# Kernel tuning notes

Measured on AMD Instinct MI355X. Metric: run time of the kernel, lower is better.

Reference implementation:

```python
import jax, jax.numpy as jnp
import numpy as np

E = 32          # n_routed_experts / num_local_experts
H = 1024        # hidden_size
I = 512         # moe_intermediate_size
G = 8           # n_group
TKG = 4         # topk_group
TOPK = 8        # num_experts_per_tok
NSH = 2         # n_shared_experts
SCALE = 2.5     # routed_scaling_factor


def setup_inputs() -> dict:
    key = jax.random.key(0)
    ks = jax.random.split(key, 10)
    s = 0.02
    return {
        "hidden_states": jax.random.normal(ks[0], (2, 1024, H), jnp.float32),
        # router: linear weight [E, H] and e_score_correction_bias [E]
        "gate_w": jax.random.normal(ks[1], (E, H), jnp.float32) * s,
        "gate_bias": jax.random.normal(ks[2], (E,), jnp.float32) * s,
        # routed experts (stacked SwiGLU weights, torch Linear layout [out, in])
        "w_gate": jax.random.normal(ks[3], (E, I, H), jnp.float32) * s,
        "w_up": jax.random.normal(ks[4], (E, I, H), jnp.float32) * s,
        "w_down": jax.random.normal(ks[5], (E, H, I), jnp.float32) * s,
        # shared experts: one MLP with intermediate = I * NSH
        "sh_gate": jax.random.normal(ks[6], (I * NSH, H), jnp.float32) * s,
        "sh_up": jax.random.normal(ks[7], (I * NSH, H), jnp.float32) * s,
        "sh_down": jax.random.normal(ks[8], (H, I * NSH), jnp.float32) * s,
    }


def reference(hidden_states, gate_w, gate_bias, w_gate, w_up, w_down,
              sh_gate, sh_up, sh_down):
    B, S, Hd = hidden_states.shape
    h = hidden_states.reshape(-1, Hd)                      # [T, H]

    # ---- router (DeepseekV3TopkRouter + route_tokens_to_experts) ----
    logits = h.astype(jnp.float32) @ gate_w.T              # [T, E]
    scores = jax.nn.sigmoid(logits)
    sc = scores + gate_bias                                # scores_for_choice
    # group score = sum of top-2 expert scores within each group
    grp = sc.reshape(-1, G, E // G)                        # [T, G, E/G]
    group_scores = jax.lax.top_k(grp, 2)[0].sum(-1)        # [T, G]
    gidx = jax.lax.top_k(group_scores, TKG)[1]             # [T, TKG]
    gmask = jnp.sum(jax.nn.one_hot(gidx, G, dtype=sc.dtype), axis=1)  # [T, G]
    smask = jnp.repeat(gmask, E // G, axis=1)              # [T, E]
    masked = jnp.where(smask > 0, sc, jnp.zeros_like(sc))  # masked_fill(~mask, 0)
    tki = jax.lax.top_k(masked, TOPK)[1]                   # [T, TOPK]
    tkw = jnp.take_along_axis(scores, tki, axis=1)         # gather raw sigmoid scores
    tkw = tkw / (tkw.sum(-1, keepdims=True) + 1e-20)       # norm_topk_prob
    tkw = tkw * SCALE

    # ---- dispatch-compute-combine (experts_forward) ----
    # combine[t, e] = sum_k tkw[t, k] * [tki[t, k] == e]
    combine = (jax.nn.one_hot(tki, E, dtype=tkw.dtype) * tkw[..., None]).sum(1)  # [T, E]
    g = jax.nn.silu(jnp.einsum('th,eih->tei', h, w_gate))  # [T, E, I]
    u = jnp.einsum('th,eih->tei', h, w_up)                 # [T, E, I]
    routed = jnp.einsum('tei,ehi->th', g * u * combine[:, :, None], w_down)  # [T, H]

    # ---- shared experts ----
    sg = jax.nn.silu(h @ sh_gate.T)
    shared = (sg * (h @ sh_up.T)) @ sh_down.T              # [T, H]

    return (routed + shared).reshape(B, S, Hd)
```

## Files before the change

### kernel.cpp

```cpp
#include <hip/hip_runtime.h>
#include <hip/hip_bf16.h>
#include <cstdint>

#define E_ 32
#define H_ 1024
#define I_ 512
#define G_ 8
#define NSH_ 2
#define SCALE_ 2.5f
#define NROUTED (E_ * I_)
#define PADCAP (16384 + E_ * 128)

typedef unsigned short u16;
using bf16x8_t = __attribute__((ext_vector_type(8))) __bf16;
using f32x4_t  = __attribute__((ext_vector_type(4))) float;

__device__ __forceinline__ u16 f2bf(float x) {
  union { float f; uint32_t u; } v; v.f = x;
  uint32_t u = v.u;
  uint32_t r = (u + 0x7fffu + ((u >> 16) & 1u)) >> 16;
  return (u16)r;
}
__device__ __forceinline__ float bf2f(u16 x) {
  union { uint32_t u; float f; } v; v.u = ((uint32_t)x) << 16; return v.f;
}

__device__ __forceinline__ void load_lds16(const void* g, void* l) {
  __builtin_amdgcn_global_load_lds(
      (const __attribute__((address_space(1))) unsigned int*)g,
      (__attribute__((address_space(3))) unsigned int*)l,
      16, 0, 0);
}

#define OFF_BU   16777216L
#define OFF_BD   33554432L
#define OFF_BSHG 50331648L
#define OFF_BSHU 51380224L
#define OFF_BSHD 52428800L
#define WBF_TOT  53477376L

#define W4_WG  4194304L
#define W4_WU  8388608L
#define W4_WD  12582912L
#define W4_SHG 12845056L
#define W4_SHU 13107200L
#define W4_TOT 13369344L
__global__ void prep_kernel(const float* __restrict__ gw, float* __restrict__ gwT,
                            int* __restrict__ counts, int* __restrict__ cursor,
                            int* __restrict__ qheads,
                            int* __restrict__ tok_list, float* __restrict__ wt_list,
                            const float* __restrict__ wg, const float* __restrict__ wu,
                            const float* __restrict__ wd, const float* __restrict__ shg,
                            const float* __restrict__ shu, const float* __restrict__ shd,
                            u16* __restrict__ wbf) {
  long i0 = (long)blockIdx.x * blockDim.x + threadIdx.x;
  if (i0 < H_ * E_) {
    int k = (int)(i0 >> 5), e = (int)(i0 & 31);
    gwT[i0] = gw[(long)e * H_ + k];
  }
  if (i0 < PADCAP) { tok_list[i0] = 0; wt_list[i0] = 0.f; }
  if (i0 < E_) { counts[i0] = 0; cursor[i0] = 0; }
  if (i0 < 2) qheads[i0] = 0;

  long stride = (long)gridDim.x * blockDim.x;
  for (long i = i0; i < W4_TOT; i += stride) {
    const float* s; long off; long dofs;
    if (i < W4_WG)       { s = wg;  off = i;            dofs = off * 4; }
    else if (i < W4_WU)  { s = wu;  off = i - W4_WG;    dofs = OFF_BU + off * 4; }
    else if (i < W4_WD)  { s = wd;  off = i - W4_WU;    dofs = OFF_BD + off * 4; }
    else if (i < W4_SHG) { s = shg; off = i - W4_WD;    dofs = OFF_BSHG + off * 4; }
    else if (i < W4_SHU) { s = shu; off = i - W4_SHG;   dofs = OFF_BSHU + off * 4; }
    else                 { s = shd; off = i - W4_SHU;   dofs = OFF_BSHD + off * 4; }
    float4 v = ((const float4*)s)[off];
    ushort4 o;
    o.x = f2bf(v.x); o.y = f2bf(v.y); o.z = f2bf(v.z); o.w = f2bf(v.w);
    *(ushort4*)(wbf + dofs) = o;
  }
}

__global__ __launch_bounds__(256) void router_kernel(
    const float* __restrict__ h, const float* __restrict__ gwT,
    const float* __restrict__ gb, u16* __restrict__ hbf,
    int* __restrict__ idx8, float* __restrict__ wt8, int* __restrict__ counts) {
  __shared__ float sh[8][H_];
  __shared__ float s_log[8][E_ + 1];
  const int tid = threadIdx.x;
  const int t0 = blockIdx.x * 8;
  #pragma unroll
  for (int c = tid; c < 8 * H_ / 4; c += 256) {
    int row = c / (H_ / 4), col = c % (H_ / 4);
    float4 v = ((const float4*)(h + (size_t)(t0 + row) * H_))[col];
    ((float4*)sh[row])[col] = v;
    ushort4 o;
    o.x = f2bf(v.x); o.y = f2bf(v.y); o.z = f2bf(v.z); o.w = f2bf(v.w);
    ((ushort4*)(hbf + (size_t)(t0 + row) * H_))[col] = o;
  }
  __syncthreads();
  {
    const int w = tid >> 6, l = tid & 63;
    const int e = l & 31, tl = w * 2 + (l >> 5);
    const float* hp = sh[tl];
    const float* wp = gwT + e;
    float acc = 0.f;
    #pragma unroll 8
    for (int k = 0; k < H_; ++k) acc += hp[k] * wp[(size_t)k * E_];
    s_log[tl][e] = acc;
  }
  __syncthreads();
  if (tid < 8) {
    const int t = t0 + tid;
    float scr[E_], sc[E_];
    #pragma unroll
    for (int e = 0; e < E_; ++e) {
      float sig = 1.f / (1.f + __expf(-s_log[tid][e]));
      scr[e] = sig;
      sc[e] = sig + gb[e];
    }
    float gs[G_];
    #pragma unroll
    for (int g = 0; g < G_; ++g) {
      float a = sc[g * 4], b = sc[g * 4 + 1], c = sc[g * 4 + 2], d = sc[g * 4 + 3];
      float hi1 = fmaxf(a, b), lo1 = fminf(a, b);
      float hi2 = fmaxf(c, d), lo2 = fminf(c, d);
      float m1 = fmaxf(hi1, hi2);
      float m2 = (hi1 >= hi2) ? fmaxf(lo1, hi2) : fmaxf(lo2, hi1);
      gs[g] = m1 + m2;
    }
    unsigned gm = 0;
    #pragma unroll
    for (int r = 0; r < 4; ++r) {
      float bv = -1e30f; int bi = 0;
      #pragma unroll
      for (int g = 0; g < G_; ++g)
        if (!(gm & (1u << g)) && gs[g] > bv) { bv = gs[g]; bi = g; }
      gm |= 1u << bi;
    }
    float msk[E_];
    #pragma unroll
    for (int e = 0; e < E_; ++e)
      msk[e] = ((gm >> (e >> 2)) & 1u) ? sc[e] : 0.f;
    unsigned um = 0; float wsum = 0.f;
    int idxs[8]; float wts[8];
    #pragma unroll
    for (int r = 0; r < 8; ++r) {
      float bv = -1e30f; int bi = 0;
      #pragma unroll
      for (int e = 0; e < E_; ++e)
        if (!(um & (1u << e)) && msk[e] > bv) { bv = msk[e]; bi = e; }
      um |= 1u << bi;
      idxs[r] = bi;
      float wv = scr[bi];
      wts[r] = wv; wsum += wv;
    }
    float inv = SCALE_ / (wsum + 1e-20f);
    #pragma unroll
    for (int r = 0; r < 8; ++r) {
      idx8[(size_t)t * 8 + r] = idxs[r];
      wt8[(size_t)t * 8 + r] = wts[r] * inv;
      atomicAdd(&counts[idxs[r]], 1);
    }
  }
}

__global__ void fill_kernel(const int* __restrict__ idx8, const float* __restrict__ wt8,
                            const int* __restrict__ counts, int* __restrict__ cursor,
                            int* __restrict__ tok_list, float* __restrict__ wt_list,
                            int* __restrict__ pair_pos, int npair) {
  int i = blockIdx.x * blockDim.x + threadIdx.x;
  if (i >= npair) return;
  int e = idx8[i];
  int offz = 0;
  for (int k = 0; k < E_; ++k) {
    if (k == e) break;
    offz += ((counts[k] + 127) >> 7) << 7;
  }
  int p = atomicAdd(&cursor[e], 1);
  int slot = offz + p;
  tok_list[slot] = i >> 3;
  wt_list[slot] = wt8[i];
  pair_pos[i] = slot;
}

__global__ __launch_bounds__(256, 2) void p1_kernel(
    const u16* __restrict__ hbf,
    const u16* __restrict__ wbf,
    const int* __restrict__ counts,
    const int* __restrict__ tok_list, const float* __restrict__ wt_list,
    int* __restrict__ qheads,
    u16* __restrict__ gu,
    u16* __restrict__ gu_sh,
    int T) {
  __shared__ u16 lsA[2][128 * 32];
  __shared__ u16 lsB0[2][128 * 32];
  __shared__ u16 lsB1[2][128 * 32];
  __shared__ int s_tok[128];
  __shared__ float s_wt[128];
  __shared__ int s_off[E_], s_ntt[E_];
  __shared__ int s_tot, s_tile;

  const int tid = threadIdx.x;
  if (tid == 0) {
    int run = 0, tot = 0;
    for (int e = 0; e < E_; ++e) {
      s_off[e] = run;
      int nt = (counts[e] + 127) >> 7;
      s_ntt[e] = nt;
      run += nt << 7;
      tot += nt * 4;
    }
    s_tot = tot + (T / 128) * 8;
  }

  const int w = tid >> 6, l = tid & 63;
  const int wr = w >> 1, wc = w & 1;
  const int lr = l & 15, lh = l >> 4;
  const int rdblk = (lh ^ ((lr >> 1) & 3)) << 3;

  const int c0 = tid, c1 = tid + 256;
  const int row0 = c0 >> 2, cb0 = c0 & 3, scb0 = cb0 ^ ((row0 >> 1) & 3);
  const int row1 = c1 >> 2, cb1 = c1 & 3, scb1 = cb1 ^ ((row1 >> 1) & 3);

  for (;;) {
    __syncthreads();
    if (tid == 0) s_tile = atomicAdd(&qheads[0], 1);
    __syncthreads();
    int q = s_tile;
    if (q >= s_tot) break;

    int z = 0, rem = q;
    for (; z < E_; ++z) { int t = s_ntt[z] * 4; if (rem < t) break; rem -= t; }
    const bool sh_e = (z == E_);
    int tt, nb;
    if (sh_e) { tt = rem >> 3; nb = rem & 7; }
    else      { tt = rem >> 2; nb = rem & 3; }
    const int off = sh_e ? 0 : s_off[z];

    if (tid < 128) {
      if (sh_e) { s_tok[tid] = tt * 128 + tid; s_wt[tid] = 1.0f; }
      else {
        int slot = off + tt * 128 + tid;
        s_tok[tid] = tok_list[slot];
        s_wt[tid] = wt_list[slot];
      }
    }
    __syncthreads();

    const u16* Bg = sh_e ? (wbf + OFF_BSHG + (size_t)(nb * 128) * H_)
                         : (wbf + ((size_t)z * I_ + nb * 128) * H_);
    const u16* Bu = sh_e ? (wbf + OFF_BSHU + (size_t)(nb * 128) * H_)
                         : (wbf + OFF_BU + ((size_t)z * I_ + nb * 128) * H_);
    const u16* A0 = hbf + (size_t)s_tok[row0] * H_ + scb0 * 8;
    const u16* A1 = hbf + (size_t)s_tok[row1] * H_ + scb1 * 8;

    f32x4_t acc0[4][4], acc1[4][4];
    #pragma unroll
    for (int m = 0; m < 4; ++m)
      #pragma unroll
      for (int n = 0; n < 4; ++n) {
        acc0[m][n] = (f32x4_t){0.f, 0.f, 0.f, 0.f};
        acc1[m][n] = (f32x4_t){0.f, 0.f, 0.f, 0.f};
      }

    auto stage = [&](int b, int k0) {
      load_lds16(A0 + k0, (char*)&lsA[b][0] + c0 * 16);
      load_lds16(A1 + k0, (char*)&lsA[b][0] + c1 * 16);
      load_lds16(Bg + (size_t)row0 * H_ + k0 + scb0 * 8, (char*)&lsB0[b][0] + c0 * 16);
      load_lds16(Bg + (size_t)row1 * H_ + k0 + scb1 * 8, (char*)&lsB0[b][0] + c1 * 16);
      load_lds16(Bu + (size_t)row0 * H_ + k0 + scb0 * 8, (char*)&lsB1[b][0] + c0 * 16);
      load_lds16(Bu + (size_t)row1 * H_ + k0 + scb1 * 8, (char*)&lsB1[b][0] + c1 * 16);
    };
    auto compute = [&](int b) {
      bf16x8_t af[4], b0f[4], b1f[4];
      #pragma unroll
      for (int m = 0; m < 4; ++m)
        af[m] = *(const bf16x8_t*)(&lsA[b][0] + (wr * 64 + m * 16 + lr) * 32 + rdblk);
      #pragma unroll
      for (int n = 0; n < 4; ++n) {
        b0f[n] = *(const bf16x8_t*)(&lsB0[b][0] + (wc * 64 + n * 16 + lr) * 32 + rdblk);
        b1f[n] = *(const bf16x8_t*)(&lsB1[b][0] + (wc * 64 + n * 16 + lr) * 32 + rdblk);
      }
      #pragma unroll
      for (int m = 0; m < 4; ++m)
        #pragma unroll
        for (int n = 0; n < 4; ++n) {
          acc0[m][n] = __builtin_amdgcn_mfma_f32_16x16x32_bf16(af[m], b0f[n], acc0[m][n], 0, 0, 0);
          acc1[m][n] = __builtin_amdgcn_mfma_f32_16x16x32_bf16(af[m], b1f[n], acc1[m][n], 0, 0, 0);
        }
    };

    stage(0, 0);
    __syncthreads();
    int cur = 0;
    #pragma unroll 1
    for (int s = 0; s < 32; ++s) {
      if (s < 31) stage(cur ^ 1, (s + 1) * 32);
      compute(cur);
      __syncthreads();
      cur ^= 1;
    }

    const int ldo = sh_e ? (I_ * NSH_) : I_;
    u16* outp = sh_e ? (gu_sh + (size_t)(tt * 128) * ldo + nb * 128)
                     : (gu + (size_t)(off + tt * 128) * ldo + nb * 128);
    #pragma unroll
    for (int m = 0; m < 4; ++m) {
      #pragma unroll
      for (int n = 0; n < 4; ++n) {
        int col = wc * 64 + n * 16 + lr;
        #pragma unroll
        for (int j = 0; j < 4; ++j) {
          int trow = wr * 64 + m * 16 + lh * 4 + j;
          float gv = acc0[m][n][j], uv = acc1[m][n][j];
          float sv = gv / (1.f + __expf(-gv));
          outp[(size_t)trow * ldo + col] = f2bf(sv * uv * s_wt[trow]);
        }
      }
    }
  }
}

__global__ __launch_bounds__(256, 3) void p2_kernel(
    const u16* __restrict__ gu, const u16* __restrict__ gu_sh,
    const u16* __restrict__ wbf,
    const int* __restrict__ counts,
    int* __restrict__ qheads,
    u16* __restrict__ part,
    u16* __restrict__ part_sh,
    int T) {
  __shared__ u16 lsA[2][128 * 32];
  __shared__ u16 lsB[2][128 * 32];
  __shared__ int s_off[E_], s_ntt[E_];
  __shared__ int s_tot, s_tile;

  const int tid = threadIdx.x;
  if (tid == 0) {
    int run = 0, tot = 0;
    for (int e = 0; e < E_; ++e) {
      s_off[e] = run;
      int nt = (counts[e] + 127) >> 7;
      s_ntt[e] = nt;
      run += nt << 7;
      tot += nt * 8;
    }
    s_tot = tot + (T / 128) * 8;
  }

  const int w = tid >> 6, l = tid & 63;
  const int wr = w >> 1, wc = w & 1;
  const int lr = l & 15, lh = l >> 4;
  const int rdblk = (lh ^ ((lr >> 1) & 3)) << 3;

  const int c0 = tid, c1 = tid + 256;
  const int row0 = c0 >> 2, cb0 = c0 & 3, scb0 = cb0 ^ ((row0 >> 1) & 3);
  const int row1 = c1 >> 2, cb1 = c1 & 3, scb1 = cb1 ^ ((row1 >> 1) & 3);

  for (;;) {
    __syncthreads();
    if (tid == 0) s_tile = atomicAdd(&qheads[1], 1);
    __syncthreads();
    int q = s_tile;
    if (q >= s_tot) break;

    int z = 0, rem = q;
    for (; z < E_; ++z) { int t = s_ntt[z] * 8; if (rem < t) break; rem -= t; }
    const bool sh_e = (z == E_);
    int tt = rem >> 3, nb = rem & 7;

    const int K = sh_e ? (I_ * NSH_) : I_;
    const int NT = K / 32;
    const u16* Ab = sh_e ? (gu_sh + (size_t)(tt * 128) * K)
                         : (gu + (size_t)(s_off[z] + tt * 128) * K);
    const u16* Bb = sh_e ? (wbf + OFF_BSHD + (size_t)(nb * 128) * K)
                         : (wbf + OFF_BD + (size_t)z * H_ * I_ + (size_t)(nb * 128) * K);
    u16* outp = sh_e ? (part_sh + (size_t)(tt * 128) * H_ + nb * 128)
                     : (part + (size_t)(s_off[z] + tt * 128) * H_ + nb * 128);

    f32x4_t acc[4][4];
    #pragma unroll
    for (int m = 0; m < 4; ++m)
      #pragma unroll
      for (int n = 0; n < 4; ++n) acc[m][n] = (f32x4_t){0.f, 0.f, 0.f, 0.f};

    auto stage = [&](int b, int k0) {
      load_lds16(Ab + (size_t)row0 * K + k0 + scb0 * 8, (char*)&lsA[b][0] + c0 * 16);
      load_lds16(Ab + (size_t)row1 * K + k0 + scb1 * 8, (char*)&lsA[b][0] + c1 * 16);
      load_lds16(Bb + (size_t)row0 * K + k0 + scb0 * 8, (char*)&lsB[b][0] + c0 * 16);
      load_lds16(Bb + (size_t)row1 * K + k0 + scb1 * 8, (char*)&lsB[b][0] + c1 * 16);
    };
    auto compute = [&](int b) {
      bf16x8_t af[4], bf[4];
      #pragma unroll
      for (int m = 0; m < 4; ++m)
        af[m] = *(const bf16x8_t*)(&lsA[b][0] + (wr * 64 + m * 16 + lr) * 32 + rdblk);
      #pragma unroll
      for (int n = 0; n < 4; ++n)
        bf[n] = *(const bf16x8_t*)(&lsB[b][0] + (wc * 64 + n * 16 + lr) * 32 + rdblk);
      #pragma unroll
      for (int m = 0; m < 4; ++m)
        #pragma unroll
        for (int n = 0; n < 4; ++n)
          acc[m][n] = __builtin_amdgcn_mfma_f32_16x16x32_bf16(af[m], bf[n], acc[m][n], 0, 0, 0);
    };

    stage(0, 0);
    __syncthreads();
    int cur = 0;
    #pragma unroll 1
    for (int s = 0; s < NT; ++s) {
      if (s < NT - 1) stage(cur ^ 1, (s + 1) * 32);
      compute(cur);
      __syncthreads();
      cur ^= 1;
    }

    #pragma unroll
    for (int m = 0; m < 4; ++m) {
      #pragma unroll
      for (int n = 0; n < 4; ++n) {
        int col = wc * 64 + n * 16 + lr;
        #pragma unroll
        for (int j = 0; j < 4; ++j) {
          int trow = wr * 64 + m * 16 + lh * 4 + j;
          outp[(size_t)trow * H_ + col] = f2bf(acc[m][n][j]);
        }
      }
    }
  }
}

__global__ void combine_kernel(const u16* __restrict__ part, const u16* __restrict__ part_sh,
                               const int* __restrict__ pair_pos, float* __restrict__ out) {
  int t = blockIdx.x;
  int h = threadIdx.x * 4;
  int pp[8];
  #pragma unroll
  for (int s = 0; s < 8; ++s) pp[s] = pair_pos[(long)t * 8 + s];
  ushort4 v = *(const ushort4*)(part_sh + (size_t)t * H_ + h);
  float a0 = bf2f(v.x), a1 = bf2f(v.y), a2 = bf2f(v.z), a3 = bf2f(v.w);
  #pragma unroll
  for (int s = 0; s < 8; ++s) {
    ushort4 u = *(const ushort4*)(part + (size_t)pp[s] * H_ + h);
    a0 += bf2f(u.x); a1 += bf2f(u.y); a2 += bf2f(u.z); a3 += bf2f(u.w);
  }
  float4 o = {a0, a1, a2, a3};
  *(float4*)(out + (size_t)t * H_ + h) = o;
}

extern "C" void kernel_launch(void* const* d_in, const int* in_sizes, int n_in,
                              void* d_out, int out_size, void* d_ws, size_t ws_size,
                              hipStream_t stream) {
  const float* hs  = (const float*)d_in[0];
  const float* gw  = (const float*)d_in[1];
  const float* gb  = (const float*)d_in[2];
  const float* wg  = (const float*)d_in[3];
  const float* wu  = (const float*)d_in[4];
  const float* wd  = (const float*)d_in[5];
  const float* shg = (const float*)d_in[6];
  const float* shu = (const float*)d_in[7];
  const float* shd = (const float*)d_in[8];
  float* out = (float*)d_out;

  const int T = in_sizes[0] / H_;

  char* ws = (char*)d_ws;
  size_t off = 0;
  auto alloc = [&](size_t bytes) {
    char* p = ws + off;
    off += (bytes + 255) & ~(size_t)255;
    return p;
  };
  int*   counts   = (int*)alloc(E_ * 4);
  int*   cursor   = (int*)alloc(E_ * 4);
  int*   qheads   = (int*)alloc(2 * 4);
  int*   idx8     = (int*)alloc((size_t)T * 8 * 4);
  float* wt8      = (float*)alloc((size_t)T * 8 * 4);
  int*   pair_pos = (int*)alloc((size_t)T * 8 * 4);
  int*   tok_list = (int*)alloc(PADCAP * 4);
  float* wt_list  = (float*)alloc(PADCAP * 4);
  float* gwT      = (float*)alloc((size_t)H_ * E_ * 4);
  u16* hbf     = (u16*)alloc((size_t)T * H_ * 2);
  u16* wbf     = (u16*)alloc((size_t)WBF_TOT * 2);
  u16* gu      = (u16*)alloc((size_t)PADCAP * I_ * 2);
  u16* gu_sh   = (u16*)alloc((size_t)T * I_ * NSH_ * 2);
  u16* part    = (u16*)alloc((size_t)PADCAP * H_ * 2);
  u16* part_sh = (u16*)alloc((size_t)T * H_ * 2);
  if (off > ws_size) return;

  hipLaunchKernelGGL(prep_kernel, dim3(4096), dim3(256), 0, stream,
                     gw, gwT, counts, cursor, qheads, tok_list, wt_list,
                     wg, wu, wd, shg, shu, shd, wbf);

  hipLaunchKernelGGL(router_kernel, dim3(T / 8), dim3(256), 0, stream,
                     hs, gwT, gb, hbf, idx8, wt8, counts);

  hipLaunchKernelGGL(fill_kernel, dim3((T * 8 + 255) / 256), dim3(256), 0, stream,
                     idx8, wt8, counts, cursor, tok_list, wt_list, pair_pos, T * 8);

  hipLaunchKernelGGL(p1_kernel, dim3(512), dim3(256), 0, stream,
                     hbf, wbf, counts, tok_list, wt_list, qheads, gu, gu_sh, T);

  hipLaunchKernelGGL(p2_kernel, dim3(768), dim3(256), 0, stream,
                     gu, gu_sh, wbf, counts, qheads, part, part_sh, T);

  hipLaunchKernelGGL(combine_kernel, dim3(T), dim3(256), 0, stream,
                     part, part_sh, pair_pos, out);
}
```

Measured before the change: 309.2 us.

## Split router into tiled split-K logits kernel and warp-parallel top-k kernel

Replaces the single router kernel with two kernels. The first computes router logits as a split-K tiled GEMM over 64-token by 128-k tiles with shared-memory staging and register blocking, writing partial sums. The second sums the partials and does grouped top-k with wavefront shuffles, one lane per expert, instead of a single serial thread per token. This is meant to remove the serial top-k bottleneck and the uncoalesced per-k weight reads, at the cost of an extra launch and a partial-logit buffer round trip.

```diff
diff --git a/kernel.cpp b/kernel.cpp
--- a/kernel.cpp
+++ b/kernel.cpp
@@ -78,87 +78,106 @@
   }
 }
 
-__global__ __launch_bounds__(256) void router_kernel(
+__global__ __launch_bounds__(256) void logits_kernel(
     const float* __restrict__ h, const float* __restrict__ gwT,
-    const float* __restrict__ gb, u16* __restrict__ hbf,
-    int* __restrict__ idx8, float* __restrict__ wt8, int* __restrict__ counts) {
-  __shared__ float sh[8][H_];
-  __shared__ float s_log[8][E_ + 1];
+    float* __restrict__ lpart,
+    u16* __restrict__ hbf, int T) {
+  __shared__ float shh[64][128];
+  __shared__ float shw[128][E_];
   const int tid = threadIdx.x;
-  const int t0 = blockIdx.x * 8;
-  #pragma unroll
-  for (int c = tid; c < 8 * H_ / 4; c += 256) {
-    int row = c / (H_ / 4), col = c % (H_ / 4);
-    float4 v = ((const float4*)(h + (size_t)(t0 + row) * H_))[col];
-    ((float4*)sh[row])[col] = v;
+  const int t0 = blockIdx.x * 64;
+  const int k0 = blockIdx.y * 128;
+  #pragma unroll
+  for (int i = 0; i < 8; ++i) {
+    int c = tid + 256 * i;
+    int row = c >> 5, col = c & 31;
+    float4 v = *(const float4*)(h + (size_t)(t0 + row) * H_ + k0 + col * 4);
+    *(float4*)(&shh[row][col * 4]) = v;
     ushort4 o;
     o.x = f2bf(v.x); o.y = f2bf(v.y); o.z = f2bf(v.z); o.w = f2bf(v.w);
-    ((ushort4*)(hbf + (size_t)(t0 + row) * H_))[col] = o;
+    *(ushort4*)(hbf + (size_t)(t0 + row) * H_ + k0 + col * 4) = o;
+  }
+  #pragma unroll
+  for (int i = 0; i < 4; ++i) {
+    int c = tid + 256 * i;
+    int row = c >> 3, col = c & 7;
+    *(float4*)(&shw[row][col * 4]) =
+        *(const float4*)(gwT + (size_t)(k0 + row) * E_ + col * 4);
   }
   __syncthreads();
-  {
-    const int w = tid >> 6, l = tid & 63;
-    const int e = l & 31, tl = w * 2 + (l >> 5);
-    const float* hp = sh[tl];
-    const float* wp = gwT + e;
-    float acc = 0.f;
-    #pragma unroll 8
-    for (int k = 0; k < H_; ++k) acc += hp[k] * wp[(size_t)k * E_];
-    s_log[tl][e] = acc;
-  }
-  __syncthreads();
-  if (tid < 8) {
-    const int t = t0 + tid;
-    float scr[E_], sc[E_];
-    #pragma unroll
-    for (int e = 0; e < E_; ++e) {
-      float sig = 1.f / (1.f + __expf(-s_log[tid][e]));
-      scr[e] = sig;
-      sc[e] = sig + gb[e];
-    }
-    float gs[G_];
-    #pragma unroll
-    for (int g = 0; g < G_; ++g) {
-      float a = sc[g * 4], b = sc[g * 4 + 1], c = sc[g * 4 + 2], d = sc[g * 4 + 3];
-      float hi1 = fmaxf(a, b), lo1 = fminf(a, b);
-      float hi2 = fmaxf(c, d), lo2 = fminf(c, d);
-      float m1 = fmaxf(hi1, hi2);
-      float m2 = (hi1 >= hi2) ? fmaxf(lo1, hi2) : fmaxf(lo2, hi1);
-      gs[g] = m1 + m2;
-    }
-    unsigned gm = 0;
-    #pragma unroll
-    for (int r = 0; r < 4; ++r) {
-      float bv = -1e30f; int bi = 0;
-      #pragma unroll
-      for (int g = 0; g < G_; ++g)
-        if (!(gm & (1u << g)) && gs[g] > bv) { bv = gs[g]; bi = g; }
-      gm |= 1u << bi;
-    }
-    float msk[E_];
-    #pragma unroll
-    for (int e = 0; e < E_; ++e)
-      msk[e] = ((gm >> (e >> 2)) & 1u) ? sc[e] : 0.f;
-    unsigned um = 0; float wsum = 0.f;
-    int idxs[8]; float wts[8];
-    #pragma unroll
-    for (int r = 0; r < 8; ++r) {
-      float bv = -1e30f; int bi = 0;
-      #pragma unroll
-      for (int e = 0; e < E_; ++e)
-        if (!(um & (1u << e)) && msk[e] > bv) { bv = msk[e]; bi = e; }
-      um |= 1u << bi;
-      idxs[r] = bi;
-      float wv = scr[bi];
-      wts[r] = wv; wsum += wv;
-    }
-    float inv = SCALE_ / (wsum + 1e-20f);
-    #pragma unroll
-    for (int r = 0; r < 8; ++r) {
-      idx8[(size_t)t * 8 + r] = idxs[r];
-      wt8[(size_t)t * 8 + r] = wts[r] * inv;
-      atomicAdd(&counts[idxs[r]], 1);
-    }
+  const int e = tid & 31;
+  const int tb = (tid >> 5) * 8;
+  float acc[8] = {0.f, 0.f, 0.f, 0.f, 0.f, 0.f, 0.f, 0.f};
+  #pragma unroll 4
+  for (int k = 0; k < 128; ++k) {
+    float wv = shw[k][e];
+    #pragma unroll
+    for (int j = 0; j < 8; ++j) acc[j] += shh[tb + j][k] * wv;
+  }
+  #pragma unroll
+  for (int j = 0; j < 8; ++j)
+    lpart[((size_t)blockIdx.y * T + (t0 + tb + j)) * E_ + e] = acc[j];
+}
+
+__global__ __launch_bounds__(256) void topk_kernel(
+    const float* __restrict__ lpart, const float* __restrict__ gb,
+    int* __restrict__ idx8, float* __restrict__ wt8, int* __restrict__ counts,
+    int T) {
+  const int tid = threadIdx.x;
+  const int l = tid & 63, wid = tid >> 6;
+  const int e = l & 31, half = l >> 5;
+  const int t = blockIdx.x * 8 + wid * 2 + half;
+
+  float lg = 0.f;
+  #pragma unroll
+  for (int s = 0; s < 8; ++s) lg += lpart[((size_t)s * T + t) * E_ + e];
+  float score = 1.f / (1.f + __expf(-lg));
+  float sc = score + gb[e];
+
+  float x1 = __shfl_xor(sc, 1);
+  float x2 = __shfl_xor(sc, 2);
+  float x3 = __shfl_xor(sc, 3);
+  float hi1 = fmaxf(sc, x1), lo1 = fminf(sc, x1);
+  float hi2 = fmaxf(x2, x3), lo2 = fminf(x2, x3);
+  float m1 = fmaxf(hi1, hi2);
+  float m2 = (hi1 >= hi2) ? fmaxf(lo1, hi2) : fmaxf(lo2, hi1);
+  float gs = m1 + m2;
+
+  float ga[8];
+  #pragma unroll
+  for (int g = 0; g < 8; ++g) ga[g] = __shfl(gs, (half << 5) + g * 4);
+  unsigned gm = 0;
+  #pragma unroll
+  for (int r = 0; r < 4; ++r) {
+    float bv = -1e30f; int bi = 0;
+    #pragma unroll
+    for (int g = 0; g < 8; ++g)
+      if (!((gm >> g) & 1u) && ga[g] > bv) { bv = ga[g]; bi = g; }
+    gm |= 1u << bi;
+  }
+  float msk = ((gm >> (e >> 2)) & 1u) ? sc : 0.f;
+
+  float wsum = 0.f, myw = 0.f;
+  int myi = 0;
+  #pragma unroll
+  for (int r = 0; r < 8; ++r) {
+    float av = msk; int ai = e;
+    #pragma unroll
+    for (int m = 16; m; m >>= 1) {
+      float ov = __shfl_xor(av, m);
+      int oi = __shfl_xor(ai, m);
+      if (ov > av || (ov == av && oi < ai)) { av = ov; ai = oi; }
+    }
+    float wscore = __shfl(score, (half << 5) + ai);
+    wsum += wscore;
+    if (e == r) { myi = ai; myw = wscore; }
+    if (e == ai) msk = 0.f;
+  }
+  float inv = SCALE_ / (wsum + 1e-20f);
+  if (e < 8) {
+    idx8[(size_t)t * 8 + e] = myi;
+    wt8[(size_t)t * 8 + e] = myw * inv;
+    atomicAdd(&counts[myi], 1);
   }
 }
 
@@ -478,6 +497,7 @@
   int*   tok_list = (int*)alloc(PADCAP * 4);
   float* wt_list  = (float*)alloc(PADCAP * 4);
   float* gwT      = (float*)alloc((size_t)H_ * E_ * 4);
+  float* lpart    = (float*)alloc((size_t)8 * T * E_ * 4);
   u16* hbf     = (u16*)alloc((size_t)T * H_ * 2);
   u16* wbf     = (u16*)alloc((size_t)WBF_TOT * 2);
   u16* gu      = (u16*)alloc((size_t)PADCAP * I_ * 2);
@@ -490,8 +510,11 @@
                      gw, gwT, counts, cursor, qheads, tok_list, wt_list,
                      wg, wu, wd, shg, shu, shd, wbf);
 
-  hipLaunchKernelGGL(router_kernel, dim3(T / 8), dim3(256), 0, stream,
-                     hs, gwT, gb, hbf, idx8, wt8, counts);
+  hipLaunchKernelGGL(logits_kernel, dim3(T / 64, 8), dim3(256), 0, stream,
+                     hs, gwT, lpart, hbf, T);
+
+  hipLaunchKernelGGL(topk_kernel, dim3(T / 8), dim3(256), 0, stream,
+                     lpart, gb, idx8, wt8, counts, T);
 
   hipLaunchKernelGGL(fill_kernel, dim3((T * 8 + 255) / 256), dim3(256), 0, stream,
                      idx8, wt8, counts, cursor, tok_list, wt_list, pair_pos, T * 8);
```

Result: faster. 268.5 us (-13.2%).
